# Kernel optimization log

Hardware: AMD Instinct MI355X
Metric: run time of the kernel (lower is better)

Reference implementation:

```python
import jax, jax.numpy as jnp
import numpy as np

C = 16          # in_channels // 4
EXP = 16        # expand_rate
SHIFTS = [1, 3, 5, 7]
BN_EPS = 1e-5

# fixed directional-difference kernels (non-trainable in the torch module)
_tmp1 = np.array([[[-1,0,0],[0,1,0],[0,0,0]],
                  [[0,-1,0],[0,1,0],[0,0,0]],
                  [[0,0,-1],[0,1,0],[0,0,0]],
                  [[0,0,0],[-1,1,0],[0,0,0]]], dtype=np.float32).reshape(4,1,3,3)
_tmp2 = _tmp1[:, :, ::-1, ::-1].copy()
K1 = jnp.asarray(np.tile(np.concatenate([_tmp1, _tmp2], 0), (C,1,1,1)))  # [8C,1,3,3]
K2 = jnp.asarray(np.tile(np.concatenate([_tmp2, _tmp1], 0), (C,1,1,1)))  # [8C,1,3,3]

def conv(x, w, groups=1, dilation=1, bias=None):
    out = jax.lax.conv_general_dilated(
        x, w, window_strides=(1,1), padding='SAME',
        rhs_dilation=(dilation, dilation),
        dimension_numbers=('NCHW','OIHW','NCHW'),
        feature_group_count=groups)
    if bias is not None:
        out = out + bias[None, :, None, None]
    return out

def setup_inputs() -> dict:
    key = jax.random.key(0)
    ks = jax.random.split(key, 20)
    B, Cin, H, W = 4, 64, 256, 256
    inp = {
        'cen': jax.random.normal(ks[0], (B, Cin, H, W), jnp.float32),
        'mas': jax.random.normal(ks[1], (B, 1, H, W), jnp.float32),
        'w_in': jax.random.normal(ks[2], (C, Cin, 1, 1), jnp.float32) * 0.1,
        'b_in': jax.random.normal(ks[3], (C,), jnp.float32) * 0.1,
        'w_c0': jax.random.normal(ks[4], (C, C, 1, 1), jnp.float32) * 0.1,
        'b_c0': jax.random.normal(ks[5], (C,), jnp.float32) * 0.1,
        'w_c1': jax.random.normal(ks[6], (C, C, 3, 3), jnp.float32) * 0.1,
        'b_c1': jax.random.normal(ks[7], (C,), jnp.float32) * 0.1,
        'w_c2': jax.random.normal(ks[8], (C, C, 5, 5), jnp.float32) * 0.05,
        'b_c2': jax.random.normal(ks[9], (C,), jnp.float32) * 0.1,
        'w_c3': jax.random.normal(ks[10], (C, C, 7, 7), jnp.float32) * 0.05,
        'b_c3': jax.random.normal(ks[11], (C,), jnp.float32) * 0.1,
        'scales1': jax.random.normal(ks[12], (4,), jnp.float32) * 0.1,
        'scales2': jax.random.normal(ks[13], (C * EXP, 8, 1, 1), jnp.float32) * 0.1,
        'scales3': jax.random.normal(ks[14], (C, EXP, 1, 1), jnp.float32) * 0.1,
        'w_base': jax.random.normal(ks[15], (C, C, 3, 3), jnp.float32) * 0.1,
        'bn_gamma': jnp.ones((C,), jnp.float32),
        'bn_beta': jnp.zeros((C,), jnp.float32),
        'bn_mean': jnp.zeros((C,), jnp.float32),
        'bn_var': jnp.ones((C,), jnp.float32),
        'w_out': jax.random.normal(ks[16], (1, C, 1, 1), jnp.float32) * 0.1,
        'b_out': jax.random.normal(ks[17], (1,), jnp.float32) * 0.1,
    }
    return inp

def reference(cen, mas, w_in, b_in, w_c0, b_c0, w_c1, b_c1, w_c2, b_c2, w_c3, b_c3,
              scales1, scales2, scales3, w_base, bn_gamma, bn_beta, bn_mean, bn_var,
              w_out, b_out):
    x = conv(cen, w_in, bias=b_in)                      # [B,C,H,W]
    k3 = jax.nn.softmax(scales2, axis=1)                # [8C*2? no: [C*EXP,8,1,1]
    k4 = jax.nn.softmax(scales3, axis=1)                # [C,EXP,1,1]
    conv_ws = [(w_c0, b_c0), (w_c1, b_c1), (w_c2, b_c2), (w_c3, b_c3)]
    outs = []
    for (wc, bc), shift in zip(conv_ws, SHIFTS):
        c = conv(x, wc, bias=bc)                        # [B,C,H,W]
        o1 = conv(c, K1, groups=C, dilation=shift)      # [B,8C,H,W]
        o2 = conv(c, K2, groups=C, dilation=shift)
        o1 = conv(o1, k3, groups=C)                     # [B,C*EXP,H,W]
        o2 = conv(o2, k3, groups=C)
        o = jnp.sort(o1 * o2, axis=2)                   # sort along H
        o = jax.nn.silu(o)
        o = conv(o, k4, groups=C)                       # [B,C,H,W]
        outs.append(o)
    outs = jnp.stack(outs, axis=-1)                     # [B,C,H,W,4]
    outs = jnp.max(outs, axis=-1) + jnp.mean(outs, axis=-1)
    # out_conv = BaseConv(3x3 conv -> BN(eval) -> SiLU) then 1x1 conv to 1 ch
    h = conv(outs, w_base)
    h = (h - bn_mean[None, :, None, None]) * jax.lax.rsqrt(bn_var + BN_EPS)[None, :, None, None]
    h = h * bn_gamma[None, :, None, None] + bn_beta[None, :, None, None]
    h = jax.nn.silu(h)
    h = conv(h, w_out, bias=b_out)
    out_mask = jax.nn.sigmoid(h)                        # [B,1,H,W]
    s = jax.nn.softmax(scales1, axis=-1)
    m = jax.nn.sigmoid(mas)
    return cen * (out_mask * m * s[0] + m * s[1] + s[2] * out_mask + s[3])
```

## Files before the change

kernel.cpp:

```cpp
#include <hip/hip_runtime.h>

#define HW 65536

constexpr int OFF_X    = 0;
constexpr int OFF_CT   = 4194304;
constexpr int OFF_MAX  = 8388608;
constexpr int OFF_SUM  = 12582912;
constexpr int P_K3  = 17039360;
constexpr int P_K3S = P_K3  + 2048;
constexpr int P_K4  = P_K3S + 2048;
constexpr int P_S1  = P_K4  + 256;
constexpr int P_BNS = P_S1  + 4;
constexpr int P_BNB = P_BNS + 16;
constexpr int P_WRI = P_BNB + 16;
constexpr int P_WR0 = P_WRI + 1024;
constexpr int P_WR1 = P_WR0 + 256;
constexpr int P_WR2 = P_WR1 + 2304;
constexpr int P_WR3 = P_WR2 + 6400;
constexpr int P_WRB = P_WR3 + 12544;
constexpr int P_K3H  = P_WRB + 2304;
constexpr int P_K3SH = P_K3H + 1024;

typedef _Float16 hv2 __attribute__((ext_vector_type(2)));

__device__ __forceinline__ int h2i(hv2 v) { return __builtin_bit_cast(int, v); }
__device__ __forceinline__ hv2 i2h(int v) { return __builtin_bit_cast(hv2, v); }

__device__ __forceinline__ hv2 pkrtz(float a, float b) {
  return __builtin_bit_cast(hv2, __builtin_amdgcn_cvt_pkrtz(a, b));
}

__device__ __forceinline__ hv2 pk_fma_n(hv2 a, hv2 b, hv2 c) {
#if __has_builtin(__builtin_elementwise_fma)
  return __builtin_elementwise_fma(a, b, c);
#else
  return a * b + c;
#endif
}

__device__ __forceinline__ hv2 pkmin(hv2 a, hv2 b) {
  hv2 d; asm("v_pk_min_f16 %0, %1, %2" : "=v"(d) : "v"(a), "v"(b)); return d;
}
__device__ __forceinline__ hv2 pkmax(hv2 a, hv2 b) {
  hv2 d; asm("v_pk_max_f16 %0, %1, %2" : "=v"(d) : "v"(a), "v"(b)); return d;
}
__device__ __forceinline__ hv2 pkmul(hv2 a, hv2 b) {
  hv2 d; asm("v_pk_mul_f16 %0, %1, %2" : "=v"(d) : "v"(a), "v"(b)); return d;
}
__device__ __forceinline__ hv2 pkfma(hv2 a, hv2 b, hv2 c) {
  hv2 d; asm("v_pk_fma_f16 %0, %1, %2, %3" : "=v"(d) : "v"(a), "v"(b), "v"(c)); return d;
}

__device__ __forceinline__ hv2 sel32(bool c, hv2 a, hv2 b) {
  return i2h(c ? h2i(a) : h2i(b));
}

template <int LMASK>
__device__ __forceinline__ int lane_xor_i(int x) {
  if constexpr (LMASK == 1) {
    return __builtin_amdgcn_mov_dpp(x, 0xB1, 0xF, 0xF, true);
  } else if constexpr (LMASK == 2) {
    return __builtin_amdgcn_mov_dpp(x, 0x4E, 0xF, 0xF, true);
  } else if constexpr (LMASK < 32) {
    return __builtin_amdgcn_ds_swizzle(x, (LMASK << 10) | 0x1F);
  } else {
    return __shfl_xor(x, LMASK, 64);
  }
}

__device__ __forceinline__ float sigmoid_fast(float x) {
  return __fdividef(1.0f, 1.0f + __expf(-x));
}

__global__ void k_prep(const float* __restrict__ w_in, const float* __restrict__ w_c0,
                       const float* __restrict__ w_c1, const float* __restrict__ w_c2,
                       const float* __restrict__ w_c3, const float* __restrict__ w_base,
                       const float* __restrict__ scales1, const float* __restrict__ scales2,
                       const float* __restrict__ scales3, const float* __restrict__ bn_gamma,
                       const float* __restrict__ bn_beta, const float* __restrict__ bn_mean,
                       const float* __restrict__ bn_var, float* __restrict__ ws) {
  int tid = threadIdx.x;
  {
    const float* srow = scales2 + tid * 8;
    float v[8]; float mx = -1e30f;
    for (int j = 0; j < 8; j++) { v[j] = srow[j]; mx = fmaxf(mx, v[j]); }
    float s = 0.f;
    for (int j = 0; j < 8; j++) { v[j] = __expf(v[j] - mx); s += v[j]; }
    float inv = 1.0f / s;
    for (int j = 0; j < 8; j++) ws[P_K3 + tid * 8 + j] = v[j] * inv;
    for (int j = 0; j < 8; j++) ws[P_K3S + tid * 8 + j] = v[(j + 4) & 7] * inv;
  }
  if (tid < 16) {
    const float* srow = scales3 + tid * 16;
    float v[16]; float mx = -1e30f;
    for (int e = 0; e < 16; e++) { v[e] = srow[e]; mx = fmaxf(mx, v[e]); }
    float s = 0.f;
    for (int e = 0; e < 16; e++) { v[e] = __expf(v[e] - mx); s += v[e]; }
    float inv = 1.0f / s;
    for (int e = 0; e < 16; e++) ws[P_K4 + tid * 16 + e] = v[e] * inv;
  }
  if (tid == 0) {
    float v[4]; float mx = -1e30f;
    for (int i = 0; i < 4; i++) { v[i] = scales1[i]; mx = fmaxf(mx, v[i]); }
    float s = 0.f;
    for (int i = 0; i < 4; i++) { v[i] = __expf(v[i] - mx); s += v[i]; }
    for (int i = 0; i < 4; i++) ws[P_S1 + i] = v[i] / s;
  }
  if (tid < 16) {
    float rs = rsqrtf(bn_var[tid] + 1e-5f);
    float sc = bn_gamma[tid] * rs;
    ws[P_BNS + tid] = sc;
    ws[P_BNB + tid] = bn_beta[tid] - bn_mean[tid] * sc;
  }
  for (int i = tid; i < 1024; i += 256) { int ci = i >> 4, co = i & 15; ws[P_WRI + i] = w_in[co * 64 + ci]; }
  {
    uint32_t* w0 = (uint32_t*)(ws + P_WR0);
    for (int i = tid; i < 128; i += 256) {
      int cp = i & 7, ci = i >> 3;
      hv2 wv;
      wv.x = (_Float16)w_c0[(2 * cp) * 16 + ci];
      wv.y = (_Float16)w_c0[(2 * cp + 1) * 16 + ci];
      w0[ci * 8 + cp] = __builtin_bit_cast(uint32_t, wv);
    }
    uint32_t* w1 = (uint32_t*)(ws + P_WR1);
    for (int i = tid; i < 1152; i += 256) {
      int cp = i & 7; int r = i >> 3; int kw = r % 3; r /= 3; int kh = r % 3; int ci = r / 3;
      hv2 wv;
      wv.x = (_Float16)w_c1[((2 * cp) * 16 + ci) * 9 + kh * 3 + kw];
      wv.y = (_Float16)w_c1[((2 * cp + 1) * 16 + ci) * 9 + kh * 3 + kw];
      w1[((ci * 3 + kh) * 3 + kw) * 8 + cp] = __builtin_bit_cast(uint32_t, wv);
    }
    uint32_t* w2 = (uint32_t*)(ws + P_WR2);
    for (int i = tid; i < 3200; i += 256) {
      int cp = i & 7; int r = i >> 3; int kw = r % 5; r /= 5; int kh = r % 5; int ci = r / 5;
      hv2 wv;
      wv.x = (_Float16)w_c2[((2 * cp) * 16 + ci) * 25 + kh * 5 + kw];
      wv.y = (_Float16)w_c2[((2 * cp + 1) * 16 + ci) * 25 + kh * 5 + kw];
      w2[((ci * 5 + kh) * 5 + kw) * 8 + cp] = __builtin_bit_cast(uint32_t, wv);
    }
    uint32_t* w3 = (uint32_t*)(ws + P_WR3);
    for (int i = tid; i < 6272; i += 256) {
      int cp = i & 7; int r = i >> 3; int kw = r % 7; r /= 7; int kh = r % 7; int ci = r / 7;
      hv2 wv;
      wv.x = (_Float16)w_c3[((2 * cp) * 16 + ci) * 49 + kh * 7 + kw];
      wv.y = (_Float16)w_c3[((2 * cp + 1) * 16 + ci) * 49 + kh * 7 + kw];
      w3[((ci * 7 + kh) * 7 + kw) * 8 + cp] = __builtin_bit_cast(uint32_t, wv);
    }
  }
  for (int i = tid; i < 2304; i += 256) {
    int co = i & 15; int r = i >> 4; int kh = r % 3; r /= 3; int kw = r % 3; int g = r / 3;
    ws[P_WRB + i] = w_base[((co * 16 + g) * 3 + kh) * 3 + kw];
  }
  __syncthreads();
  uint32_t* k3h  = (uint32_t*)(ws + P_K3H);
  uint32_t* k3sh = (uint32_t*)(ws + P_K3SH);
  for (int i = tid; i < 1024; i += 256) {
    int g = i >> 6, p = (i >> 3) & 7, j = i & 7;
    hv2 wv, wvs;
    wv.x  = (_Float16)ws[P_K3 + g * 128 + (2 * p) * 8 + j];
    wv.y  = (_Float16)ws[P_K3 + g * 128 + (2 * p + 1) * 8 + j];
    wvs.x = (_Float16)ws[P_K3S + g * 128 + (2 * p) * 8 + j];
    wvs.y = (_Float16)ws[P_K3S + g * 128 + (2 * p + 1) * 8 + j];
    k3h[i]  = __builtin_bit_cast(uint32_t, wv);
    k3sh[i] = __builtin_bit_cast(uint32_t, wvs);
  }
}

__global__ __launch_bounds__(256) void k_in(const float* __restrict__ cen,
                                            const float* __restrict__ b_in,
                                            const float* __restrict__ ws,
                                            float* __restrict__ xT) {
  __shared__ float ldst[16 * 16 * 17];
  int tid = threadIdx.x;
  int b = blockIdx.z;
  int hbase = blockIdx.y * 16, wbase = blockIdx.x * 16;
  int ty = tid >> 4, tx = tid & 15;
  const float* wri = ws + P_WRI;
  float acc[16];
#pragma unroll
  for (int co = 0; co < 16; co++) acc[co] = b_in[co];
  const float* cp = cen + b * 64 * HW + (hbase + ty) * 256 + wbase + tx;
#pragma unroll 4
  for (int ci = 0; ci < 64; ci++) {
    float v = cp[ci * HW];
#pragma unroll
    for (int co = 0; co < 16; co++) acc[co] = fmaf(wri[ci * 16 + co], v, acc[co]);
  }
#pragma unroll
  for (int co = 0; co < 16; co++) ldst[(co * 16 + tx) * 17 + ty] = acc[co];
  __syncthreads();
  int wy = tid >> 4, hx = tid & 15;
#pragma unroll
  for (int ci = 0; ci < 16; ci++) {
    xT[((b * 16 + ci) << 16) + (wbase + wy) * 256 + hbase + hx] =
        ldst[(ci * 16 + wy) * 17 + hx];
  }
}

template <int KS>
__global__ __launch_bounds__(256) void k_conv(const float* __restrict__ xT,
                                              const float* __restrict__ bias,
                                              const uint32_t* __restrict__ wrh,
                                              float* __restrict__ cT) {
  constexpr int P = KS / 2;
  const int tid = threadIdx.x;
  const int lane = tid & 63;
  const int wv = (blockIdx.x << 2) + (tid >> 6);
  const int hseg = wv & 3;
  const int w = (wv >> 2) & 255;
  const int b = wv >> 10;
  const int hbase = hseg << 6;
  const float* xb = xT + ((b * 16) << 16);

  hv2 acc[8];
#pragma unroll
  for (int cp = 0; cp < 8; cp++) {
    hv2 bv;
    bv.x = (_Float16)bias[2 * cp];
    bv.y = (_Float16)bias[2 * cp + 1];
    acc[cp] = bv;
  }

#pragma unroll 2
  for (int ci = 0; ci < 16; ci++) {
#pragma unroll
    for (int kw = 0; kw < KS; kw++) {
      const int wc = w + kw - P;
      if ((unsigned)wc >= 256u) continue;
      const float* col = xb + (ci << 16) + (wc << 8);
      const int h0 = hbase + lane - P;
      float v0 = ((unsigned)h0 < 256u) ? col[h0] : 0.0f;
      float v1 = 0.0f;
      if (P > 0) {
        const int h1 = hbase + 64 - P + lane;
        v1 = (lane < 2 * P && (unsigned)h1 < 256u) ? col[h1] : 0.0f;
      }
#pragma unroll
      for (int kh = 0; kh < KS; kh++) {
        float tv;
        if (P == 0) {
          tv = v0;
        } else {
          const int s = lane + kh;
          float t0 = __shfl(v0, s & 63, 64);
          float t1 = __shfl(v1, (s - 64) & 63, 64);
          tv = (s < 64) ? t0 : t1;
        }
        const hv2 tp = pkrtz(tv, tv);
        const uint32_t* wp = wrh + ((ci * KS + kh) * KS + kw) * 8;
#pragma unroll
        for (int cp = 0; cp < 8; cp++)
          acc[cp] = pk_fma_n(i2h((int)wp[cp]), tp, acc[cp]);
      }
    }
  }
  float* o = cT + ((b * 16) << 16) + (w << 8) + hbase + lane;
#pragma unroll
  for (int cp = 0; cp < 8; cp++) {
    o[(2 * cp) << 16] = (float)acc[cp].x;
    o[(2 * cp + 1) << 16] = (float)acc[cp].y;
  }
}

__device__ __forceinline__ void ce_pair_h(hv2& a, hv2& b, bool up) {
  hv2 lo = pkmin(a, b);
  hv2 hi = pkmax(a, b);
  a = sel32(up, lo, hi);
  b = sel32(up, hi, lo);
}

template <int SIZE, int DIST>
__device__ __forceinline__ void stage_x_h(hv2 v[4], int i0) {
  const bool keepmin = (((i0 & DIST) == 0) == ((i0 & SIZE) == 0));
#pragma unroll
  for (int r = 0; r < 4; r++) {
    hv2 pv = i2h(lane_xor_i<(DIST >> 2)>(h2i(v[r])));
    v[r] = sel32(keepmin, pkmin(v[r], pv), pkmax(v[r], pv));
  }
}

template <int SIZE>
__device__ __forceinline__ void stage_d21_h(hv2 v[4], int i0) {
  bool up = ((i0 & SIZE) == 0);
  ce_pair_h(v[0], v[2], up); ce_pair_h(v[1], v[3], up);
  ce_pair_h(v[0], v[1], up); ce_pair_h(v[2], v[3], up);
}

__device__ __forceinline__ void sort256h(hv2 v[4], int lane) {
  int i0 = lane << 2;
  ce_pair_h(v[0], v[1], true); ce_pair_h(v[2], v[3], false);
  stage_d21_h<4>(v, i0);
  stage_x_h<8, 4>(v, i0); stage_d21_h<8>(v, i0);
  stage_x_h<16, 8>(v, i0); stage_x_h<16, 4>(v, i0); stage_d21_h<16>(v, i0);
  stage_x_h<32, 16>(v, i0); stage_x_h<32, 8>(v, i0); stage_x_h<32, 4>(v, i0); stage_d21_h<32>(v, i0);
  stage_x_h<64, 32>(v, i0); stage_x_h<64, 16>(v, i0); stage_x_h<64, 8>(v, i0); stage_x_h<64, 4>(v, i0); stage_d21_h<64>(v, i0);
  stage_x_h<128, 64>(v, i0); stage_x_h<128, 32>(v, i0); stage_x_h<128, 16>(v, i0); stage_x_h<128, 8>(v, i0); stage_x_h<128, 4>(v, i0); stage_d21_h<128>(v, i0);
  stage_x_h<256, 128>(v, i0); stage_x_h<256, 64>(v, i0); stage_x_h<256, 32>(v, i0); stage_x_h<256, 16>(v, i0); stage_x_h<256, 8>(v, i0); stage_x_h<256, 4>(v, i0); stage_d21_h<256>(v, i0);
}

template <int DIL>
__global__ __launch_bounds__(256) void k_branch(const float* __restrict__ cT,
                                                const float* __restrict__ ws,
                                                float* __restrict__ maxb,
                                                float* __restrict__ sumb,
                                                int initFlag) {
  const int tid = threadIdx.x;
  const int lane = tid & 63;
  const int wid = __builtin_amdgcn_readfirstlane(tid >> 6);
  const int wv = (blockIdx.x << 2) + wid;
  const int w = wv & 255;
  const int g = (wv >> 8) & 15;
  const int b = wv >> 12;
  const float* base = cT + ((b * 16 + g) << 16);

  float vals[3][3][4];
#pragma unroll
  for (int wi = 0; wi < 3; ++wi) {
    const int wc = w + (wi - 1) * DIL;
    const bool wok = ((unsigned)wc < 256u);
    const float* col = base + (wok ? wc : 0) * 256;
#pragma unroll
    for (int si = 0; si < 3; ++si) {
#pragma unroll
      for (int r = 0; r < 4; ++r) {
        const int h = lane + (r << 6) + (si - 1) * DIL;
        const bool ok = wok && ((unsigned)h < 256u);
        vals[wi][si][r] = ok ? col[h] : 0.0f;
      }
    }
  }
  hv2 ddh[8][4];
#pragma unroll
  for (int r = 0; r < 4; ++r) {
    const float c0 = vals[1][1][r];
    float d0 = c0 - vals[0][0][r];
    float d1 = c0 - vals[1][0][r];
    float d2 = c0 - vals[2][0][r];
    float d3 = c0 - vals[0][1][r];
    float d4 = c0 - vals[2][2][r];
    float d5 = c0 - vals[1][2][r];
    float d6 = c0 - vals[0][2][r];
    float d7 = c0 - vals[2][1][r];
    ddh[0][r] = pkrtz(d0, d0);
    ddh[1][r] = pkrtz(d1, d1);
    ddh[2][r] = pkrtz(d2, d2);
    ddh[3][r] = pkrtz(d3, d3);
    ddh[4][r] = pkrtz(d4, d4);
    ddh[5][r] = pkrtz(d5, d5);
    ddh[6][r] = pkrtz(d6, d6);
    ddh[7][r] = pkrtz(d7, d7);
  }
  float out[4] = {0.f, 0.f, 0.f, 0.f};
  const uint32_t* k3h  = (const uint32_t*)(ws + P_K3H)  + g * 64;
  const uint32_t* k3sh = (const uint32_t*)(ws + P_K3SH) + g * 64;
  const float* k4p = ws + P_K4 + g * 16;
#pragma unroll 1
  for (int p = 0; p < 8; ++p) {
    hv2 t[4];
    hv2 wk3[8], wk3s[8];
#pragma unroll
    for (int j = 0; j < 8; ++j) {
      wk3[j]  = i2h((int)k3h[p * 8 + j]);
      wk3s[j] = i2h((int)k3sh[p * 8 + j]);
    }
#pragma unroll
    for (int r = 0; r < 4; ++r) {
      hv2 o1 = pkmul(wk3[0], ddh[0][r]);
      hv2 o2 = pkmul(wk3s[0], ddh[0][r]);
#pragma unroll
      for (int j = 1; j < 8; ++j) {
        o1 = pkfma(wk3[j], ddh[j][r], o1);
        o2 = pkfma(wk3s[j], ddh[j][r], o2);
      }
      t[r] = pkmul(o1, o2);
    }
    sort256h(t, lane);
    const float k4a = k4p[2 * p], k4b = k4p[2 * p + 1];
#pragma unroll
    for (int r = 0; r < 4; ++r) {
      const float va = (float)t[r].x;
      const float vb = (float)t[r].y;
      out[r] = fmaf(k4a, va * sigmoid_fast(va), out[r]);
      out[r] = fmaf(k4b, vb * sigmoid_fast(vb), out[r]);
    }
  }
  const int obase = (((b * 16 + g) << 8) + w) * 256 + (lane << 2);
  float4 o4 = make_float4(out[0], out[1], out[2], out[3]);
  float4* mp = (float4*)(maxb + obase);
  float4* sp = (float4*)(sumb + obase);
  if (initFlag) {
    *mp = o4;
    *sp = o4;
  } else {
    float4 m = *mp;
    m.x = fmaxf(m.x, o4.x); m.y = fmaxf(m.y, o4.y);
    m.z = fmaxf(m.z, o4.z); m.w = fmaxf(m.w, o4.w);
    *mp = m;
    float4 s = *sp;
    s.x += o4.x; s.y += o4.y; s.z += o4.z; s.w += o4.w;
    *sp = s;
  }
}

__global__ __launch_bounds__(256) void k_tail(const float* __restrict__ maxb,
                                              const float* __restrict__ sumb,
                                              const float* __restrict__ ws,
                                              const float* __restrict__ cen,
                                              const float* __restrict__ mas,
                                              const float* __restrict__ w_out,
                                              const float* __restrict__ b_out,
                                              float* __restrict__ out) {
  __shared__ float lds[16 * 18 * 18];
  __shared__ float ldsf[256];
  int tid = threadIdx.x;
  int b = blockIdx.z;
  int wbase = blockIdx.x * 16, hbase = blockIdx.y * 16;
  const float* mb = maxb + (b * 16) * HW;
  const float* sb = sumb + (b * 16) * HW;
  for (int i = tid; i < 16 * 18 * 18; i += 256) {
    int g = i / 324; int r = i % 324; int xx = r / 18, yy = r % 18;
    int wq = wbase + xx - 1, hq = hbase + yy - 1;
    float v = 0.0f;
    if (wq >= 0 && wq < 256 && hq >= 0 && hq < 256) {
      int idx = g * HW + wq * 256 + hq;
      v = mb[idx] + 0.25f * sb[idx];
    }
    lds[i] = v;
  }
  __syncthreads();
  int xw = tid >> 4, yh = tid & 15;
  float acc[16] = {0.f, 0.f, 0.f, 0.f, 0.f, 0.f, 0.f, 0.f,
                   0.f, 0.f, 0.f, 0.f, 0.f, 0.f, 0.f, 0.f};
  for (int g = 0; g < 16; g++) {
#pragma unroll
    for (int kw = 0; kw < 3; kw++) {
#pragma unroll
      for (int kh = 0; kh < 3; kh++) {
        float v = lds[g * 324 + (xw + kw) * 18 + (yh + kh)];
        const float* wp = ws + P_WRB + ((g * 3 + kw) * 3 + kh) * 16;
#pragma unroll
        for (int co = 0; co < 16; co++) acc[co] = fmaf(wp[co], v, acc[co]);
      }
    }
  }
  float mo = b_out[0];
#pragma unroll
  for (int co = 0; co < 16; co++) {
    float z = acc[co] * ws[P_BNS + co] + ws[P_BNB + co];
    float sl = z * sigmoid_fast(z);
    mo = fmaf(w_out[co], sl, mo);
  }
  float mk = sigmoid_fast(mo);
  ldsf[yh * 16 + xw] = mk;
  __syncthreads();
  {
    int yy = tid >> 4, xx = tid & 15;
    float mkv = ldsf[yy * 16 + xx];
    float m = sigmoid_fast(mas[b * HW + (hbase + yy) * 256 + wbase + xx]);
    float s0 = ws[P_S1], s1 = ws[P_S1 + 1], s2 = ws[P_S1 + 2], s3 = ws[P_S1 + 3];
    float f = mkv * m * s0 + m * s1 + s2 * mkv + s3;
    ldsf[yy * 16 + xx] = f;
  }
  __syncthreads();
  const float* cb = cen + b * 64 * HW;
  float* ob = out + b * 64 * HW;
#pragma unroll 4
  for (int it = 0; it < 16; ++it) {
    int flat = it * 256 + tid;
    int ci = flat >> 6;
    int rr = flat & 63;
    int yy = rr >> 2, wq = rr & 3;
    const float* fr = &ldsf[yy * 16 + wq * 4];
    float4 f4 = make_float4(fr[0], fr[1], fr[2], fr[3]);
    int addr = ci * HW + (hbase + yy) * 256 + wbase + wq * 4;
    const float4 c4 = *(const float4*)(cb + addr);
    float4 o4;
    o4.x = c4.x * f4.x; o4.y = c4.y * f4.y; o4.z = c4.z * f4.z; o4.w = c4.w * f4.w;
    *(float4*)(ob + addr) = o4;
  }
}

extern "C" void kernel_launch(void* const* d_in, const int* in_sizes, int n_in,
                              void* d_out, int out_size, void* d_ws, size_t ws_size,
                              hipStream_t stream) {
  (void)in_sizes; (void)n_in; (void)out_size; (void)ws_size;
  const float* cen = (const float*)d_in[0];
  const float* mas = (const float*)d_in[1];
  const float* w_in = (const float*)d_in[2];
  const float* b_in = (const float*)d_in[3];
  const float* w_c0 = (const float*)d_in[4];
  const float* b_c0 = (const float*)d_in[5];
  const float* w_c1 = (const float*)d_in[6];
  const float* b_c1 = (const float*)d_in[7];
  const float* w_c2 = (const float*)d_in[8];
  const float* b_c2 = (const float*)d_in[9];
  const float* w_c3 = (const float*)d_in[10];
  const float* b_c3 = (const float*)d_in[11];
  const float* scales1 = (const float*)d_in[12];
  const float* scales2 = (const float*)d_in[13];
  const float* scales3 = (const float*)d_in[14];
  const float* w_base = (const float*)d_in[15];
  const float* bn_gamma = (const float*)d_in[16];
  const float* bn_beta = (const float*)d_in[17];
  const float* bn_mean = (const float*)d_in[18];
  const float* bn_var = (const float*)d_in[19];
  const float* w_out = (const float*)d_in[20];
  const float* b_out = (const float*)d_in[21];
  float* ws = (float*)d_ws;
  float* out = (float*)d_out;

  float* xT = ws + OFF_X;
  float* cT = ws + OFF_CT;
  float* maxb = ws + OFF_MAX;
  float* sumb = ws + OFF_SUM;

  k_prep<<<1, 256, 0, stream>>>(w_in, w_c0, w_c1, w_c2, w_c3, w_base, scales1, scales2,
                                scales3, bn_gamma, bn_beta, bn_mean, bn_var, ws);
  k_in<<<dim3(16, 16, 4), 256, 0, stream>>>(cen, b_in, ws, xT);

  k_conv<1><<<1024, 256, 0, stream>>>(xT, b_c0, (const uint32_t*)(ws + P_WR0), cT);
  k_branch<1><<<4096, 256, 0, stream>>>(cT, ws, maxb, sumb, 1);
  k_conv<3><<<1024, 256, 0, stream>>>(xT, b_c1, (const uint32_t*)(ws + P_WR1), cT);
  k_branch<3><<<4096, 256, 0, stream>>>(cT, ws, maxb, sumb, 0);
  k_conv<5><<<1024, 256, 0, stream>>>(xT, b_c2, (const uint32_t*)(ws + P_WR2), cT);
  k_branch<5><<<4096, 256, 0, stream>>>(cT, ws, maxb, sumb, 0);
  k_conv<7><<<1024, 256, 0, stream>>>(xT, b_c3, (const uint32_t*)(ws + P_WR3), cT);
  k_branch<7><<<4096, 256, 0, stream>>>(cT, ws, maxb, sumb, 0);

  k_tail<<<dim3(16, 16, 4), 256, 0, stream>>>(maxb, sumb, ws, cen, mas, w_out, b_out, out);
}
```

Baseline: 939.3 us.

## Factor swapped k3 weights into sum/difference bases to halve FMAs

Exploits the half-swap symmetry between the k3 and shifted k3 weights: o1 and o2 are rewritten as s+d and s-d, where s and d are four-term dot products over the summed and differenced directional features. This cuts the per-pixel packed FMA count from 16 to 8 and halves the weight loads, at the cost of a few extra adds and changed fp16 rounding. The DPP paths for xor-1/2 lane swaps are also dropped in favour of ds_swizzle, which may add latency in the sort.

```diff
diff --git a/kernel.cpp b/kernel.cpp
--- a/kernel.cpp
+++ b/kernel.cpp
@@ -18,8 +18,8 @@
 constexpr int P_WR2 = P_WR1 + 2304;
 constexpr int P_WR3 = P_WR2 + 6400;
 constexpr int P_WRB = P_WR3 + 12544;
-constexpr int P_K3H  = P_WRB + 2304;
-constexpr int P_K3SH = P_K3H + 1024;
+constexpr int P_K3U = P_WRB + 2304;
+constexpr int P_K3V = P_K3U + 512;
 
 typedef _Float16 hv2 __attribute__((ext_vector_type(2)));
 
@@ -57,11 +57,7 @@
 
 template <int LMASK>
 __device__ __forceinline__ int lane_xor_i(int x) {
-  if constexpr (LMASK == 1) {
-    return __builtin_amdgcn_mov_dpp(x, 0xB1, 0xF, 0xF, true);
-  } else if constexpr (LMASK == 2) {
-    return __builtin_amdgcn_mov_dpp(x, 0x4E, 0xF, 0xF, true);
-  } else if constexpr (LMASK < 32) {
+  if constexpr (LMASK < 32) {
     return __builtin_amdgcn_ds_swizzle(x, (LMASK << 10) | 0x1F);
   } else {
     return __shfl_xor(x, LMASK, 64);
@@ -88,7 +84,6 @@
     for (int j = 0; j < 8; j++) { v[j] = __expf(v[j] - mx); s += v[j]; }
     float inv = 1.0f / s;
     for (int j = 0; j < 8; j++) ws[P_K3 + tid * 8 + j] = v[j] * inv;
-    for (int j = 0; j < 8; j++) ws[P_K3S + tid * 8 + j] = v[(j + 4) & 7] * inv;
   }
   if (tid < 16) {
     const float* srow = scales3 + tid * 16;
@@ -152,17 +147,19 @@
     ws[P_WRB + i] = w_base[((co * 16 + g) * 3 + kh) * 3 + kw];
   }
   __syncthreads();
-  uint32_t* k3h  = (uint32_t*)(ws + P_K3H);
-  uint32_t* k3sh = (uint32_t*)(ws + P_K3SH);
-  for (int i = tid; i < 1024; i += 256) {
-    int g = i >> 6, p = (i >> 3) & 7, j = i & 7;
-    hv2 wv, wvs;
-    wv.x  = (_Float16)ws[P_K3 + g * 128 + (2 * p) * 8 + j];
-    wv.y  = (_Float16)ws[P_K3 + g * 128 + (2 * p + 1) * 8 + j];
-    wvs.x = (_Float16)ws[P_K3S + g * 128 + (2 * p) * 8 + j];
-    wvs.y = (_Float16)ws[P_K3S + g * 128 + (2 * p + 1) * 8 + j];
-    k3h[i]  = __builtin_bit_cast(uint32_t, wv);
-    k3sh[i] = __builtin_bit_cast(uint32_t, wvs);
+  uint32_t* k3u = (uint32_t*)(ws + P_K3U);
+  uint32_t* k3v = (uint32_t*)(ws + P_K3V);
+  for (int i = tid; i < 512; i += 256) {
+    int g = i >> 5, p = (i >> 2) & 7, j = i & 3;
+    const float* r0 = ws + P_K3 + g * 128 + (2 * p) * 8;
+    const float* r1 = ws + P_K3 + g * 128 + (2 * p + 1) * 8;
+    hv2 wu, wv;
+    wu.x = (_Float16)((r0[j] + r0[j + 4]) * 0.5f);
+    wu.y = (_Float16)((r1[j] + r1[j + 4]) * 0.5f);
+    wv.x = (_Float16)((r0[j] - r0[j + 4]) * 0.5f);
+    wv.y = (_Float16)((r1[j] - r1[j + 4]) * 0.5f);
+    k3u[i] = __builtin_bit_cast(uint32_t, wu);
+    k3v[i] = __builtin_bit_cast(uint32_t, wv);
   }
 }
 
@@ -329,7 +326,7 @@
       }
     }
   }
-  hv2 ddh[8][4];
+  hv2 uh[4][4], vh[4][4];
 #pragma unroll
   for (int r = 0; r < 4; ++r) {
     const float c0 = vals[1][1][r];
@@ -341,38 +338,39 @@
     float d5 = c0 - vals[1][2][r];
     float d6 = c0 - vals[0][2][r];
     float d7 = c0 - vals[2][1][r];
-    ddh[0][r] = pkrtz(d0, d0);
-    ddh[1][r] = pkrtz(d1, d1);
-    ddh[2][r] = pkrtz(d2, d2);
-    ddh[3][r] = pkrtz(d3, d3);
-    ddh[4][r] = pkrtz(d4, d4);
-    ddh[5][r] = pkrtz(d5, d5);
-    ddh[6][r] = pkrtz(d6, d6);
-    ddh[7][r] = pkrtz(d7, d7);
+    uh[0][r] = pkrtz(d0 + d4, d0 + d4);
+    uh[1][r] = pkrtz(d1 + d5, d1 + d5);
+    uh[2][r] = pkrtz(d2 + d6, d2 + d6);
+    uh[3][r] = pkrtz(d3 + d7, d3 + d7);
+    vh[0][r] = pkrtz(d0 - d4, d0 - d4);
+    vh[1][r] = pkrtz(d1 - d5, d1 - d5);
+    vh[2][r] = pkrtz(d2 - d6, d2 - d6);
+    vh[3][r] = pkrtz(d3 - d7, d3 - d7);
   }
   float out[4] = {0.f, 0.f, 0.f, 0.f};
-  const uint32_t* k3h  = (const uint32_t*)(ws + P_K3H)  + g * 64;
-  const uint32_t* k3sh = (const uint32_t*)(ws + P_K3SH) + g * 64;
+  const uint32_t* k3u = (const uint32_t*)(ws + P_K3U) + g * 32;
+  const uint32_t* k3v = (const uint32_t*)(ws + P_K3V) + g * 32;
   const float* k4p = ws + P_K4 + g * 16;
 #pragma unroll 1
   for (int p = 0; p < 8; ++p) {
     hv2 t[4];
-    hv2 wk3[8], wk3s[8];
-#pragma unroll
-    for (int j = 0; j < 8; ++j) {
-      wk3[j]  = i2h((int)k3h[p * 8 + j]);
-      wk3s[j] = i2h((int)k3sh[p * 8 + j]);
+    hv2 wu[4], wvv[4];
+#pragma unroll
+    for (int j = 0; j < 4; ++j) {
+      wu[j]  = i2h((int)k3u[p * 4 + j]);
+      wvv[j] = i2h((int)k3v[p * 4 + j]);
     }
 #pragma unroll
     for (int r = 0; r < 4; ++r) {
-      hv2 o1 = pkmul(wk3[0], ddh[0][r]);
-      hv2 o2 = pkmul(wk3s[0], ddh[0][r]);
-#pragma unroll
-      for (int j = 1; j < 8; ++j) {
-        o1 = pkfma(wk3[j], ddh[j][r], o1);
-        o2 = pkfma(wk3s[j], ddh[j][r], o2);
-      }
-      t[r] = pkmul(o1, o2);
+      hv2 s = pkmul(wu[0], uh[0][r]);
+      s = pkfma(wu[1], uh[1][r], s);
+      s = pkfma(wu[2], uh[2][r], s);
+      s = pkfma(wu[3], uh[3][r], s);
+      hv2 d = pkmul(wvv[0], vh[0][r]);
+      d = pkfma(wvv[1], vh[1][r], d);
+      d = pkfma(wvv[2], vh[2][r], d);
+      d = pkfma(wvv[3], vh[3][r], d);
+      t[r] = pkmul(s + d, s - d);
     }
     sort256h(t, lane);
     const float k4a = k4p[2 * p], k4b = k4p[2 * p + 1];
```

New measurement: 884.9 us. 5.8% less time.
